# Kernel tuning notes

Hardware: AMD Instinct MI355X
Metric: run time of the kernel (lower is better)

## Reference

```python
import jax, jax.numpy as jnp
import numpy as np

# Config constants (from init_kwargs)
RADIUS_UPDATE_RATE = 0.01
MIN_RADIUS = 0.1
MAX_RADIUS = 2.0
EPS = 1e-6


def _finite(x, fallback):
    """nan/inf guard: replace non-finite entries with fallback (same math as torch.where(isnan|isinf,...))."""
    bad = jnp.isnan(x) | jnp.isinf(x)
    return jnp.where(bad, fallback, x)


def _compute_score(r, causal=True):
    """QuantumAttention.compute_score: relu'd 2-D dot-product interaction,
    causal mask, row-normalized. r: [B,S,2] -> score: [B,S,S]."""
    raw = jnp.einsum('bse,bte->bst', r, r)          # thin bmm, inner dim 2
    score = jax.nn.relu(raw)
    if causal:
        S = r.shape[1]
        mask = jnp.tril(jnp.ones((S, S), dtype=bool))
        score = jnp.where(mask[None, :, :], score, 0.0)
    denom = jnp.clip(jnp.sum(score, axis=-1, keepdims=True), EPS, None)
    return score / denom


def setup_inputs() -> dict:
    key = jax.random.key(0)
    k1, k2 = jax.random.split(key)
    B, S = 4, 4096
    r_embed = jax.random.normal(k1, (B, S, 2), dtype=jnp.float32)
    # dt in a realistic (dt_scale .. dt_max) range
    dt = jax.random.uniform(k2, (B,), dtype=jnp.float32, minval=1e-4, maxval=1e-2)
    return {"r_embed": r_embed, "dt": dt}


def reference(r_embed, dt):
    # Heun-Euler integration step with radius rescale.
    dt_e = dt[:, None, None]                         # [B,1,1]

    # Stage 1 (k1)
    score = _compute_score(r_embed, causal=True)     # [B,S,S]
    context = jnp.einsum('bst,bte->bse', score, r_embed)
    k1 = _finite(dt_e * context, 0.0)
    r_mid = _finite(r_embed + k1, r_embed)

    # Stage 2 (k2)
    score_mid = _compute_score(r_mid, causal=True)
    context_mid = jnp.einsum('bst,bte->bse', score_mid, r_mid)
    k2 = _finite(dt_e * context_mid, 0.0)

    # Final update + radius adjustment
    r_new = r_embed + 0.5 * (k1 + k2)
    new_radius = jnp.clip(jnp.linalg.norm(r_new, axis=-1, keepdims=True), EPS, None)
    radius_adjustment = jnp.sum(score, axis=-1, keepdims=True) * RADIUS_UPDATE_RATE
    adjusted_radius = jnp.clip(new_radius + radius_adjustment, MIN_RADIUS, MAX_RADIUS)
    scale_factor = adjusted_radius / new_radius
    r_final = r_new * scale_factor
    r_final = _finite(r_final, r_embed)
    return r_final, score
```

## Files before the change

kernel.cpp:

```cpp
#include <hip/hip_runtime.h>
#include <math.h>


#define S_LEN 4096
#define ROWS  16384
#define BLK   256
#define EPSF  1e-6f
#define RATE  0.01f
#define MINR  0.1f
#define MAXR  2.0f

typedef float vf4 __attribute__((ext_vector_type(4)));

__device__ __forceinline__ void wave_red3(float &a, float &b, float &c) {
    #pragma unroll
    for (int off = 32; off > 0; off >>= 1) {
        a += __shfl_down(a, off);
        b += __shfl_down(b, off);
        c += __shfl_down(c, off);
    }
}


__global__ __launch_bounds__(BLK) void k_pass1(
    const float2* __restrict__ r_in,
    const float* __restrict__ dt_in,
    float* __restrict__ ws,
    float* __restrict__ score_out)
{
    const int lane = threadIdx.x & 63;
    const int row  = (blockIdx.x << 2) + (threadIdx.x >> 6);
    const int b = row >> 12;
    const int s = row & (S_LEN - 1);
    const float2* rb  = r_in + ((size_t)b << 12);
    const vf4*    rb4 = (const vf4*)rb;
    const float2  rs  = rb[s];

    float dsum = 0.f, nx = 0.f, ny = 0.f;
    for (int i = lane; 2*i <= s; i += 64) {
        vf4 p = rb4[i];
        float d0 = fmaxf(rs.x * p.x + rs.y * p.y, 0.f);
        dsum += d0; nx = fmaf(d0, p.x, nx); ny = fmaf(d0, p.y, ny);
        if (2*i + 1 <= s) {
            float d1 = fmaxf(rs.x * p.z + rs.y * p.w, 0.f);
            dsum += d1; nx = fmaf(d1, p.z, nx); ny = fmaf(d1, p.w, ny);
        }
    }
    wave_red3(dsum, nx, ny);
    const float D  = __shfl(dsum, 0);
    const float Nx = __shfl(nx, 0);
    const float Ny = __shfl(ny, 0);

    const float dc  = fmaxf(D, EPSF);
    const float inv = 1.f / dc;
    if (lane == 0) {
        const float dtb = dt_in[b];
        float k1x = dtb * Nx * inv;
        float k1y = dtb * Ny * inv;
        if (!isfinite(k1x)) k1x = 0.f;
        if (!isfinite(k1y)) k1y = 0.f;
        float rmx = rs.x + k1x, rmy = rs.y + k1y;
        if (!isfinite(rmx)) rmx = rs.x;
        if (!isfinite(rmy)) rmy = rs.y;
        float* rmid = ws;
        float* k1w  = ws + 2 * ROWS;
        float* s1w  = ws + 4 * ROWS;
        rmid[2*row]   = rmx; rmid[2*row+1] = rmy;
        k1w[2*row]    = k1x; k1w[2*row+1]  = k1y;
        s1w[row]      = D * inv;
    }

    const float isx = rs.x * inv, isy = rs.y * inv;
    vf4* orow = (vf4*)(score_out + (size_t)row * S_LEN);
    #pragma unroll 4
    for (int j = 0; j < 16; j++) {
        const int i4 = lane + (j << 6);
        const int t  = i4 << 2;
        vf4 v = {0.f, 0.f, 0.f, 0.f};
        if (t <= s) {
            vf4 p01 = rb4[2*i4];
            vf4 p23 = rb4[2*i4 + 1];
            v.x = fmaxf(isx * p01.x + isy * p01.y, 0.f);
            v.y = (t + 1 <= s) ? fmaxf(isx * p01.z + isy * p01.w, 0.f) : 0.f;
            v.z = (t + 2 <= s) ? fmaxf(isx * p23.x + isy * p23.y, 0.f) : 0.f;
            v.w = (t + 3 <= s) ? fmaxf(isx * p23.z + isy * p23.w, 0.f) : 0.f;
        }
        __builtin_nontemporal_store(v, orow + i4);
    }
}

__global__ __launch_bounds__(BLK) void k_pass2(
    const float2* __restrict__ r_in,
    const float* __restrict__ dt_in,
    const float* __restrict__ ws,
    float* __restrict__ rfinal_out)
{
    const int lane = threadIdx.x & 63;
    const int row  = (blockIdx.x << 2) + (threadIdx.x >> 6);
    const int b = row >> 12;
    const int s = row & (S_LEN - 1);
    const float2* rm  = ((const float2*)ws) + ((size_t)b << 12);
    const vf4*    rm4 = (const vf4*)rm;
    const float2  rs  = rm[s];

    float dsum = 0.f, nx = 0.f, ny = 0.f;
    for (int i = lane; 2*i <= s; i += 64) {
        vf4 p = rm4[i];
        float d0 = fmaxf(rs.x * p.x + rs.y * p.y, 0.f);
        dsum += d0; nx = fmaf(d0, p.x, nx); ny = fmaf(d0, p.y, ny);
        if (2*i + 1 <= s) {
            float d1 = fmaxf(rs.x * p.z + rs.y * p.w, 0.f);
            dsum += d1; nx = fmaf(d1, p.z, nx); ny = fmaf(d1, p.w, ny);
        }
    }
    wave_red3(dsum, nx, ny);
    if (lane == 0) {
        const float* k1w = ws + 2 * ROWS;
        const float* s1w = ws + 4 * ROWS;
        const float dc = fmaxf(dsum, EPSF);
        const float dtb = dt_in[b];
        float k2x = dtb * nx / dc;
        float k2y = dtb * ny / dc;
        if (!isfinite(k2x)) k2x = 0.f;
        if (!isfinite(k2y)) k2y = 0.f;
        const float2 r0 = r_in[row];
        const float k1x = k1w[2*row], k1y = k1w[2*row+1];
        const float rnx = r0.x + 0.5f * (k1x + k2x);
        const float rny = r0.y + 0.5f * (k1y + k2y);
        const float nr = fmaxf(sqrtf(rnx*rnx + rny*rny), EPSF);
        const float ar = fminf(fmaxf(nr + s1w[row] * RATE, MINR), MAXR);
        const float sc = ar / nr;
        float fx = rnx * sc, fy = rny * sc;
        if (!isfinite(fx)) fx = r0.x;
        if (!isfinite(fy)) fy = r0.y;
        rfinal_out[2*row]   = fx;
        rfinal_out[2*row+1] = fy;
    }
}

extern "C" void kernel_launch(void* const* d_in, const int* in_sizes, int n_in,
                              void* d_out, int out_size, void* d_ws, size_t ws_size,
                              hipStream_t stream) {
    const float2* r_in  = (const float2*)d_in[0];
    const float*  dt_in = (const float*)d_in[1];
    float* out = (float*)d_out;
    float* ws  = (float*)d_ws;

    float* rfinal_out = out;
    float* score_out  = out + (size_t)2 * ROWS;

    hipLaunchKernelGGL(k_pass1, dim3(ROWS / 4), dim3(BLK), 0, stream,
                       r_in, dt_in, ws, score_out);
    hipLaunchKernelGGL(k_pass2, dim3(ROWS / 4), dim3(BLK), 0, stream,
                       r_in, dt_in, ws, rfinal_out);
}
```

Baseline: 287.7 us.

## Split score write into a separate tiled kernel reusing column data across rows

Moves the score-matrix write out of the per-row reduction kernel into its own kernel. Each block handles a 16-row by 1024-column tile, loading column embeddings once and reusing them across rows, and fully masked tiles just store zeros without computing. The reduction kernel now also saves each row's inverse denominator so the score kernel can normalise. Plain stores replace nontemporal stores, and the extra launch and the workspace round-trip are added costs.

```diff
diff --git a/kernel.cpp b/kernel.cpp
--- a/kernel.cpp
+++ b/kernel.cpp
@@ -5,6 +5,8 @@
 #define S_LEN 4096
 #define ROWS  16384
 #define BLK   256
+#define TR    16
+#define TC    1024
 #define EPSF  1e-6f
 #define RATE  0.01f
 #define MINR  0.1f
@@ -22,11 +24,10 @@
 }
 
 
-__global__ __launch_bounds__(BLK) void k_pass1(
+__global__ __launch_bounds__(BLK) void k_red1(
     const float2* __restrict__ r_in,
     const float* __restrict__ dt_in,
-    float* __restrict__ ws,
-    float* __restrict__ score_out)
+    float* __restrict__ ws)
 {
     const int lane = threadIdx.x & 63;
     const int row  = (blockIdx.x << 2) + (threadIdx.x >> 6);
@@ -47,49 +48,74 @@
         }
     }
     wave_red3(dsum, nx, ny);
-    const float D  = __shfl(dsum, 0);
-    const float Nx = __shfl(nx, 0);
-    const float Ny = __shfl(ny, 0);
-
-    const float dc  = fmaxf(D, EPSF);
-    const float inv = 1.f / dc;
     if (lane == 0) {
+        const float D   = dsum;
+        const float inv = 1.f / fmaxf(D, EPSF);
         const float dtb = dt_in[b];
-        float k1x = dtb * Nx * inv;
-        float k1y = dtb * Ny * inv;
+        float k1x = dtb * nx * inv;
+        float k1y = dtb * ny * inv;
         if (!isfinite(k1x)) k1x = 0.f;
         if (!isfinite(k1y)) k1y = 0.f;
         float rmx = rs.x + k1x, rmy = rs.y + k1y;
         if (!isfinite(rmx)) rmx = rs.x;
         if (!isfinite(rmy)) rmy = rs.y;
-        float* rmid = ws;
-        float* k1w  = ws + 2 * ROWS;
-        float* s1w  = ws + 4 * ROWS;
-        rmid[2*row]   = rmx; rmid[2*row+1] = rmy;
-        k1w[2*row]    = k1x; k1w[2*row+1]  = k1y;
-        s1w[row]      = D * inv;
-    }
-
-    const float isx = rs.x * inv, isy = rs.y * inv;
-    vf4* orow = (vf4*)(score_out + (size_t)row * S_LEN);
-    #pragma unroll 4
-    for (int j = 0; j < 16; j++) {
-        const int i4 = lane + (j << 6);
-        const int t  = i4 << 2;
-        vf4 v = {0.f, 0.f, 0.f, 0.f};
-        if (t <= s) {
-            vf4 p01 = rb4[2*i4];
-            vf4 p23 = rb4[2*i4 + 1];
-            v.x = fmaxf(isx * p01.x + isy * p01.y, 0.f);
-            v.y = (t + 1 <= s) ? fmaxf(isx * p01.z + isy * p01.w, 0.f) : 0.f;
-            v.z = (t + 2 <= s) ? fmaxf(isx * p23.x + isy * p23.y, 0.f) : 0.f;
-            v.w = (t + 3 <= s) ? fmaxf(isx * p23.z + isy * p23.w, 0.f) : 0.f;
-        }
-        __builtin_nontemporal_store(v, orow + i4);
+        ws[2*row]            = rmx;  ws[2*row+1]          = rmy;
+        ws[2*ROWS + 2*row]   = k1x;  ws[2*ROWS + 2*row+1] = k1y;
+        ws[4*ROWS + row]     = D * inv;
+        ws[5*ROWS + row]     = inv;
     }
 }
 
-__global__ __launch_bounds__(BLK) void k_pass2(
+__global__ __launch_bounds__(BLK) void k_score(
+    const float2* __restrict__ r_in,
+    const float* __restrict__ ws,
+    float* __restrict__ score_out)
+{
+    const int ct   = blockIdx.x;
+    const int row0 = blockIdx.y * TR;
+    const int b    = row0 >> 12;
+    const int s0   = row0 & (S_LEN - 1);
+    const int t0   = ct << 10;
+    const int c    = t0 + (threadIdx.x << 2);
+    float* out0 = score_out + (size_t)row0 * S_LEN + c;
+
+    if (t0 > s0 + TR - 1) {
+        const vf4 z = {0.f, 0.f, 0.f, 0.f};
+        #pragma unroll
+        for (int rr = 0; rr < TR; rr++)
+            *(vf4*)(out0 + (size_t)rr * S_LEN) = z;
+        return;
+    }
+
+    const vf4* rb4 = (const vf4*)(r_in + ((size_t)b << 12));
+    const vf4 p01 = rb4[c >> 1];
+    const vf4 p23 = rb4[(c >> 1) + 1];
+    const float2* rrow = r_in;
+    const float*  invw = ws + 5 * ROWS;
+
+    const bool nomask = (t0 + TC - 1) <= s0;
+    #pragma unroll
+    for (int rr = 0; rr < TR; rr++) {
+        const float2 rv = rrow[row0 + rr];
+        const float  iv = invw[row0 + rr];
+        const float sx = rv.x * iv, sy = rv.y * iv;
+        vf4 v;
+        v.x = fmaxf(sx * p01.x + sy * p01.y, 0.f);
+        v.y = fmaxf(sx * p01.z + sy * p01.w, 0.f);
+        v.z = fmaxf(sx * p23.x + sy * p23.y, 0.f);
+        v.w = fmaxf(sx * p23.z + sy * p23.w, 0.f);
+        if (!nomask) {
+            const int s = s0 + rr;
+            v.x = (c     <= s) ? v.x : 0.f;
+            v.y = (c + 1 <= s) ? v.y : 0.f;
+            v.z = (c + 2 <= s) ? v.z : 0.f;
+            v.w = (c + 3 <= s) ? v.w : 0.f;
+        }
+        *(vf4*)(out0 + (size_t)rr * S_LEN) = v;
+    }
+}
+
+__global__ __launch_bounds__(BLK) void k_red2(
     const float2* __restrict__ r_in,
     const float* __restrict__ dt_in,
     const float* __restrict__ ws,
@@ -115,8 +141,6 @@
     }
     wave_red3(dsum, nx, ny);
     if (lane == 0) {
-        const float* k1w = ws + 2 * ROWS;
-        const float* s1w = ws + 4 * ROWS;
         const float dc = fmaxf(dsum, EPSF);
         const float dtb = dt_in[b];
         float k2x = dtb * nx / dc;
@@ -124,11 +148,11 @@
         if (!isfinite(k2x)) k2x = 0.f;
         if (!isfinite(k2y)) k2y = 0.f;
         const float2 r0 = r_in[row];
-        const float k1x = k1w[2*row], k1y = k1w[2*row+1];
+        const float k1x = ws[2*ROWS + 2*row], k1y = ws[2*ROWS + 2*row+1];
         const float rnx = r0.x + 0.5f * (k1x + k2x);
         const float rny = r0.y + 0.5f * (k1y + k2y);
         const float nr = fmaxf(sqrtf(rnx*rnx + rny*rny), EPSF);
-        const float ar = fminf(fmaxf(nr + s1w[row] * RATE, MINR), MAXR);
+        const float ar = fminf(fmaxf(nr + ws[4*ROWS + row] * RATE, MINR), MAXR);
         const float sc = ar / nr;
         float fx = rnx * sc, fy = rny * sc;
         if (!isfinite(fx)) fx = r0.x;
@@ -149,8 +173,10 @@
     float* rfinal_out = out;
     float* score_out  = out + (size_t)2 * ROWS;
 
-    hipLaunchKernelGGL(k_pass1, dim3(ROWS / 4), dim3(BLK), 0, stream,
-                       r_in, dt_in, ws, score_out);
-    hipLaunchKernelGGL(k_pass2, dim3(ROWS / 4), dim3(BLK), 0, stream,
+    hipLaunchKernelGGL(k_red1, dim3(ROWS / 4), dim3(BLK), 0, stream,
+                       r_in, dt_in, ws);
+    hipLaunchKernelGGL(k_score, dim3(S_LEN / TC, ROWS / TR), dim3(BLK), 0, stream,
+                       r_in, ws, score_out);
+    hipLaunchKernelGGL(k_red2, dim3(ROWS / 4), dim3(BLK), 0, stream,
                        r_in, dt_in, ws, rfinal_out);
 }
```

Result: no change. 292.0 us (+1.5%).
